# Kernel optimization log

Measured on AMD Instinct MI355X. Metric: run time of the kernel, lower is better.

Reference implementation:

```python
import jax, jax.numpy as jnp
import numpy as np

N_NODES = 100000
N_EDGES = 800000
N_GRAPHS = 64
D_IN = 128
D_H = 256
D_MID = 64
D_OUT = 3


def _sage_conv(x, src, dst, Wl, bl, Wr, n_nodes):
    # PyG SAGEConv (mean aggr): out = lin_l(mean_{j in N(i)} x_j) + lin_r(x_i)
    msg_sum = jax.ops.segment_sum(x[src], dst, num_segments=n_nodes)   # [N, d]
    deg = jax.ops.segment_sum(jnp.ones((src.shape[0],), x.dtype), dst,
                              num_segments=n_nodes)                     # [N]
    mean = msg_sum / jnp.maximum(deg, 1.0)[:, None]
    return mean @ Wl + bl + x @ Wr


def setup_inputs() -> dict:
    key = jax.random.key(0)
    ks = jax.random.split(key, 16)
    s = 0.05
    inp = {
        "x": jax.random.normal(ks[0], (N_NODES, D_IN), dtype=jnp.float32),
        "edge_index": jax.random.randint(ks[1], (2, N_EDGES), 0, N_NODES, dtype=jnp.int32),
        "batch": jnp.sort(jax.random.randint(ks[2], (N_NODES,), 0, N_GRAPHS, dtype=jnp.int32)),
        # conv1
        "W1l": jax.random.normal(ks[3], (D_IN, D_H), dtype=jnp.float32) * s,
        "b1l": jnp.zeros((D_H,), jnp.float32),
        "W1r": jax.random.normal(ks[4], (D_IN, D_H), dtype=jnp.float32) * s,
        # conv2
        "W2l": jax.random.normal(ks[5], (D_H, D_H), dtype=jnp.float32) * s,
        "b2l": jnp.zeros((D_H,), jnp.float32),
        "W2r": jax.random.normal(ks[6], (D_H, D_H), dtype=jnp.float32) * s,
        # conv3
        "W3l": jax.random.normal(ks[7], (D_H, D_H), dtype=jnp.float32) * s,
        "b3l": jnp.zeros((D_H,), jnp.float32),
        "W3r": jax.random.normal(ks[8], (D_H, D_H), dtype=jnp.float32) * s,
        # head
        "Wlin1": jax.random.normal(ks[9], (D_H, D_MID), dtype=jnp.float32) * s,
        "blin1": jnp.zeros((D_MID,), jnp.float32),
        "Wlin2": jax.random.normal(ks[10], (D_MID, D_OUT), dtype=jnp.float32) * s,
        "blin2": jnp.zeros((D_OUT,), jnp.float32),
    }
    return inp


def reference(x, edge_index, batch, W1l, b1l, W1r, W2l, b2l, W2r,
              W3l, b3l, W3r, Wlin1, blin1, Wlin2, blin2):
    src, dst = edge_index[0], edge_index[1]
    h = jnp.tanh(_sage_conv(x, src, dst, W1l, b1l, W1r, N_NODES))
    h = jnp.tanh(_sage_conv(h, src, dst, W2l, b2l, W2r, N_NODES))
    h = _sage_conv(h, src, dst, W3l, b3l, W3r, N_NODES)
    pooled = jax.ops.segment_max(h, batch, num_segments=N_GRAPHS)  # [G, 256]
    pooled = jnp.where(jnp.isneginf(pooled), 0.0, pooled)  # empty segments -> 0
    # dropout_rate = 0.0 -> identity
    h = jnp.tanh(pooled @ Wlin1 + blin1)
    return h @ Wlin2 + blin2
```

## Files before the change

### kernel.cpp

```cpp
#include <hip/hip_runtime.h>

#define N_NODES 100000
#define N_PAD   100224
#define N_EDGES 800000
#define N_GRAPHS 64
#define D_IN 128
#define D_H 256

typedef __attribute__((ext_vector_type(8))) short bf16x8;
typedef __attribute__((ext_vector_type(8))) unsigned short u16x8;
typedef __attribute__((ext_vector_type(4))) float f32x4;

__device__ inline float bf2f(unsigned short u) {
    union { unsigned u32; float f; } x;
    x.u32 = ((unsigned)u) << 16;
    return x.f;
}
__device__ inline unsigned short f2bf(float f) {
    unsigned u = __float_as_uint(f);
    if ((u & 0x7fffffffu) > 0x7f800000u) return (unsigned short)0x7fc0;
    unsigned r = ((u >> 16) & 1u) + 0x7fffu;
    return (unsigned short)((u + r) >> 16);
}

__device__ inline unsigned enc_f32(float f) {
    unsigned u = __float_as_uint(f);
    return (u & 0x80000000u) ? ~u : (u | 0x80000000u);
}
__device__ inline float dec_f32(unsigned u) {
    unsigned v = (u & 0x80000000u) ? (u & 0x7FFFFFFFu) : ~u;
    return __uint_as_float(v);
}
#define ENC_NEG_INF 0x007FFFFFu

#define GLOAD_LDS16(g, l)                                                     \
    __builtin_amdgcn_global_load_lds(                                         \
        (const __attribute__((address_space(1))) unsigned int*)(g),           \
        (__attribute__((address_space(3))) unsigned int*)(l), 16, 0, 0)

__global__ void k_init_counts(int* __restrict__ counts) {
    int i = blockIdx.x * blockDim.x + threadIdx.x;
    if (i < N_NODES) counts[i] = 0;
}

__global__ void k_count(const int* __restrict__ dst, int* __restrict__ counts) {
    int e = blockIdx.x * blockDim.x + threadIdx.x;
    if (e < N_EDGES) atomicAdd(&counts[dst[e]], 1);
}

__global__ void k_scan_block(const int* __restrict__ counts, int* __restrict__ excl,
                             int* __restrict__ bsums) {
    __shared__ int sh[1024];
    int tid = threadIdx.x;
    int i = blockIdx.x * 1024 + tid;
    int v = (i < N_NODES) ? counts[i] : 0;
    sh[tid] = v;
    __syncthreads();
    for (int off = 1; off < 1024; off <<= 1) {
        int t = (tid >= off) ? sh[tid - off] : 0;
        __syncthreads();
        sh[tid] += t;
        __syncthreads();
    }
    if (i < N_NODES) excl[i] = sh[tid] - v;
    if (tid == 1023) bsums[blockIdx.x] = sh[1023];
}

__global__ void k_scan_top(int* __restrict__ bsums, int nb) {
    __shared__ int sh[128];
    int tid = threadIdx.x;
    int v = (tid < nb) ? bsums[tid] : 0;
    sh[tid] = v;
    __syncthreads();
    for (int off = 1; off < 128; off <<= 1) {
        int t = (tid >= off) ? sh[tid - off] : 0;
        __syncthreads();
        sh[tid] += t;
        __syncthreads();
    }
    if (tid < nb) bsums[tid] = sh[tid] - v;
}

__global__ void k_scan_finish(const int* __restrict__ excl, const int* __restrict__ bsums,
                              const int* __restrict__ counts, int* __restrict__ indptr,
                              int* __restrict__ cursor, float* __restrict__ deg_inv) {
    int i = blockIdx.x * blockDim.x + threadIdx.x;
    if (i < N_NODES) {
        int p = excl[i] + bsums[i >> 10];
        indptr[i] = p;
        cursor[i] = p;
        deg_inv[i] = 1.0f / fmaxf((float)counts[i], 1.0f);
        if (i == 0) indptr[N_NODES] = N_EDGES;
    }
}

__global__ void k_fill(const int* __restrict__ src, const int* __restrict__ dst,
                       int* __restrict__ cursor, int* __restrict__ eidx) {
    int e = blockIdx.x * blockDim.x + threadIdx.x;
    if (e < N_EDGES) {
        int pos = atomicAdd(&cursor[dst[e]], 1);
        eidx[pos] = src[e];
    }
}

__global__ void k_x2bf(const float* __restrict__ x, unsigned short* __restrict__ hx) {
    const int total = N_NODES * D_IN / 4;
    for (int i = blockIdx.x * blockDim.x + threadIdx.x; i < total;
         i += gridDim.x * blockDim.x) {
        float4 v = reinterpret_cast<const float4*>(x)[i];
        ushort4 o;
        o.x = f2bf(v.x); o.y = f2bf(v.y); o.z = f2bf(v.z); o.w = f2bf(v.w);
        reinterpret_cast<ushort4*>(hx)[i] = o;
    }
}

template <int K>
__global__ void k_wt(const float* __restrict__ W, unsigned short* __restrict__ Wt) {
    int idx = blockIdx.x * blockDim.x + threadIdx.x;
    if (idx < K * 256) {
        int k = idx >> 8, n = idx & 255;
        Wt[n * K + k] = f2bf(W[idx]);
    }
}

template <bool IN_F32>
__global__ void k_agg(const void* __restrict__ hin, const int* __restrict__ indptr,
                      const int* __restrict__ eidx, const float* __restrict__ deg_inv,
                      unsigned short* __restrict__ mean) {
    constexpr int D = IN_F32 ? 128 : 256;
    constexpr int C = IN_F32 ? 4 : 8;
    int wid = (blockIdx.x * blockDim.x + threadIdx.x) >> 6;
    int lane = threadIdx.x & 63;
    int nw = (gridDim.x * blockDim.x) >> 6;
    int half = lane >> 5;
    int l = lane & 31;
    for (int node = wid; node < N_NODES; node += nw) {
        int beg = indptr[node], end = indptr[node + 1];
        float acc[C] = {};
        for (int e = beg + half; e < end; e += 2) {
            int s = eidx[e];
            if (IN_F32) {
                float4 v = reinterpret_cast<const float4*>((const float*)hin + (size_t)s * D)[l];
                acc[0] += v.x; acc[1] += v.y; acc[2] += v.z; acc[3] += v.w;
            } else {
                u16x8 v = reinterpret_cast<const u16x8*>((const unsigned short*)hin + (size_t)s * D)[l];
#pragma unroll
                for (int j = 0; j < 8; ++j) acc[j] += bf2f((unsigned short)v[j]);
            }
        }
#pragma unroll
        for (int i = 0; i < C; ++i) acc[i] += __shfl_xor(acc[i], 32);
        if (lane < 32) {
            float inv = deg_inv[node];
            unsigned short* orow = mean + (size_t)node * D;
            if (IN_F32) {
                ushort4 o;
                o.x = f2bf(acc[0] * inv); o.y = f2bf(acc[1] * inv);
                o.z = f2bf(acc[2] * inv); o.w = f2bf(acc[3] * inv);
                reinterpret_cast<ushort4*>(orow)[l] = o;
            } else {
                u16x8 o;
#pragma unroll
                for (int j = 0; j < 8; ++j) o[j] = f2bf(acc[j] * inv);
                reinterpret_cast<u16x8*>(orow)[l] = o;
            }
        }
    }
}

template <int K, bool TANH, bool POOL>
__global__ __launch_bounds__(512)
void k_xform(const unsigned short* __restrict__ A0, const unsigned short* __restrict__ A1,
             const unsigned short* __restrict__ Bt0, const unsigned short* __restrict__ Bt1,
             const float* __restrict__ bias,
             unsigned short* __restrict__ out,
             const int* __restrict__ batch, unsigned* __restrict__ pooled) {
    __shared__ unsigned short Al[128 * 32];
    __shared__ unsigned short Bl[256 * 32];

    const int tid = threadIdx.x;
    const int lane = tid & 63;
    const int wid = tid >> 6;
    const int wr = wid >> 2;
    const int wc = wid & 3;
    const int m0 = blockIdx.x * 128;

    f32x4 acc[4][4] = {};

    const int lrow = lane >> 2;
    const int lk8 = (lane & 3) * 8;

#pragma unroll
    for (int slab = 0; slab < 2; ++slab) {
        const unsigned short* As = slab ? A1 : A0;
        const unsigned short* Bs = slab ? Bt1 : Bt0;
        for (int k0 = 0; k0 < K; k0 += 32) {
            __syncthreads();
            GLOAD_LDS16(As + (size_t)(m0 + wid * 16 + lrow) * K + k0 + lk8, &Al[wid * 512]);
#pragma unroll
            for (int cc = 0; cc < 2; ++cc) {
                int c = wid * 2 + cc;
                GLOAD_LDS16(Bs + (size_t)(c * 16 + lrow) * K + k0 + lk8, &Bl[c * 512]);
            }
            asm volatile("s_waitcnt vmcnt(0)" ::: "memory");
            __syncthreads();

            bf16x8 af[4], bfr[4];
#pragma unroll
            for (int f = 0; f < 4; ++f) {
                af[f] = *reinterpret_cast<const bf16x8*>(
                    &Al[(wr * 64 + f * 16 + (lane & 15)) * 32 + (lane >> 4) * 8]);
                bfr[f] = *reinterpret_cast<const bf16x8*>(
                    &Bl[(wc * 64 + f * 16 + (lane & 15)) * 32 + (lane >> 4) * 8]);
            }
#pragma unroll
            for (int fi = 0; fi < 4; ++fi)
#pragma unroll
                for (int fj = 0; fj < 4; ++fj)
                    acc[fi][fj] = __builtin_amdgcn_mfma_f32_16x16x32_bf16(
                        af[fi], bfr[fj], acc[fi][fj], 0, 0, 0);
        }
    }

    const int rbase = m0 + wr * 64 + (lane >> 4) * 4;
    const int cbase = wc * 64 + (lane & 15);
    if (POOL) {
#pragma unroll
        for (int fj = 0; fj < 4; ++fj) {
            int col = cbase + fj * 16;
            float bcol = bias[col];
            int curg = -1;
            float curmax = 0.f;
#pragma unroll
            for (int fi = 0; fi < 4; ++fi) {
#pragma unroll
                for (int r = 0; r < 4; ++r) {
                    int row = rbase + fi * 16 + r;
                    if (row >= N_NODES) continue;
                    float v = acc[fi][fj][r] + bcol;
                    if (TANH) v = tanhf(v);
                    int g = batch[row];
                    if (g != curg) {
                        if (curg >= 0) atomicMax(&pooled[curg * 256 + col], enc_f32(curmax));
                        curg = g;
                        curmax = v;
                    } else {
                        curmax = fmaxf(curmax, v);
                    }
                }
            }
            if (curg >= 0) atomicMax(&pooled[curg * 256 + col], enc_f32(curmax));
        }
    } else {
#pragma unroll
        for (int fi = 0; fi < 4; ++fi) {
#pragma unroll
            for (int fj = 0; fj < 4; ++fj) {
                int col = cbase + fj * 16;
                float bcol = bias[col];
#pragma unroll
                for (int r = 0; r < 4; ++r) {
                    int row = rbase + fi * 16 + r;
                    if (row >= N_NODES) continue;
                    float v = acc[fi][fj][r] + bcol;
                    if (TANH) v = tanhf(v);
                    out[(size_t)row * 256 + col] = f2bf(v);
                }
            }
        }
    }
}

__global__ void k_pool_init(unsigned* __restrict__ pooled) {
    int i = blockIdx.x * blockDim.x + threadIdx.x;
    if (i < N_GRAPHS * 256) pooled[i] = ENC_NEG_INF;
}

__global__ void k_head(const unsigned* __restrict__ pooled,
                       const float* __restrict__ W1, const float* __restrict__ b1,
                       const float* __restrict__ W2, const float* __restrict__ b2,
                       float* __restrict__ out) {
    __shared__ float p[256];
    __shared__ float hm[64];
    int g = blockIdx.x;
    int t = threadIdx.x;
    for (int k = t; k < 256; k += 64) {
        unsigned u = pooled[g * 256 + k];
        p[k] = (u == ENC_NEG_INF) ? 0.0f : dec_f32(u);
    }
    __syncthreads();
    float a = b1[t];
    for (int k = 0; k < 256; ++k) a += p[k] * W1[k * 64 + t];
    hm[t] = tanhf(a);
    __syncthreads();
    if (t < 3) {
        float o = b2[t];
        for (int m = 0; m < 64; ++m) o += hm[m] * W2[m * 3 + t];
        out[g * 3 + t] = o;
    }
}

extern "C" void kernel_launch(void* const* d_in, const int* in_sizes, int n_in,
                              void* d_out, int out_size, void* d_ws, size_t ws_size,
                              hipStream_t stream) {
    const float* x     = (const float*)d_in[0];
    const int*   ei    = (const int*)d_in[1];
    const int*   src   = ei;
    const int*   dst   = ei + N_EDGES;
    const int*   batch = (const int*)d_in[2];
    const float* W1l = (const float*)d_in[3];
    const float* b1l = (const float*)d_in[4];
    const float* W1r = (const float*)d_in[5];
    const float* W2l = (const float*)d_in[6];
    const float* b2l = (const float*)d_in[7];
    const float* W2r = (const float*)d_in[8];
    const float* W3l = (const float*)d_in[9];
    const float* b3l = (const float*)d_in[10];
    const float* W3r = (const float*)d_in[11];
    const float* Wlin1 = (const float*)d_in[12];
    const float* blin1 = (const float*)d_in[13];
    const float* Wlin2 = (const float*)d_in[14];
    const float* blin2 = (const float*)d_in[15];
    float* out = (float*)d_out;

    char* base = (char*)d_ws;
    size_t off = 0;
    auto alloc = [&](size_t bytes) { char* p = base + off; off += (bytes + 255) & ~(size_t)255; return (void*)p; };
    int*   counts  = (int*)alloc(N_NODES * 4);
    int*   indptr  = (int*)alloc((N_NODES + 1) * 4);
    int*   cursor  = (int*)alloc(N_NODES * 4);
    int*   excl    = (int*)alloc(N_NODES * 4);
    int*   bsums   = (int*)alloc(128 * 4);
    float* deg_inv = (float*)alloc(N_NODES * 4);
    unsigned* pooled = (unsigned*)alloc(N_GRAPHS * 256 * 4);
    int*   eidx    = (int*)alloc(N_EDGES * 4);
    unsigned short* Wt1l = (unsigned short*)alloc(256 * 128 * 2);
    unsigned short* Wt1r = (unsigned short*)alloc(256 * 128 * 2);
    unsigned short* Wt2l = (unsigned short*)alloc(256 * 256 * 2);
    unsigned short* Wt2r = (unsigned short*)alloc(256 * 256 * 2);
    unsigned short* Wt3l = (unsigned short*)alloc(256 * 256 * 2);
    unsigned short* Wt3r = (unsigned short*)alloc(256 * 256 * 2);
    unsigned short* M   = (unsigned short*)alloc((size_t)N_PAD * 256 * 2);
    unsigned short* hA  = (unsigned short*)alloc((size_t)N_PAD * 256 * 2);
    unsigned short* hxB = (unsigned short*)alloc((size_t)N_PAD * 256 * 2);
    unsigned short* hx = hxB;
    unsigned short* hB = hxB;

    const int NB_SCAN = (N_NODES + 1023) / 1024;

    k_init_counts<<<(N_NODES + 255) / 256, 256, 0, stream>>>(counts);
    k_count<<<(N_EDGES + 255) / 256, 256, 0, stream>>>(dst, counts);
    k_scan_block<<<NB_SCAN, 1024, 0, stream>>>(counts, excl, bsums);
    k_scan_top<<<1, 128, 0, stream>>>(bsums, NB_SCAN);
    k_scan_finish<<<(N_NODES + 255) / 256, 256, 0, stream>>>(excl, bsums, counts, indptr, cursor, deg_inv);
    k_fill<<<(N_EDGES + 255) / 256, 256, 0, stream>>>(src, dst, cursor, eidx);

    k_x2bf<<<2048, 256, 0, stream>>>(x, hx);
    k_wt<128><<<(128 * 256 + 255) / 256, 256, 0, stream>>>(W1l, Wt1l);
    k_wt<128><<<(128 * 256 + 255) / 256, 256, 0, stream>>>(W1r, Wt1r);
    k_wt<256><<<(256 * 256 + 255) / 256, 256, 0, stream>>>(W2l, Wt2l);
    k_wt<256><<<(256 * 256 + 255) / 256, 256, 0, stream>>>(W2r, Wt2r);
    k_wt<256><<<(256 * 256 + 255) / 256, 256, 0, stream>>>(W3l, Wt3l);
    k_wt<256><<<(256 * 256 + 255) / 256, 256, 0, stream>>>(W3r, Wt3r);
    k_pool_init<<<(N_GRAPHS * 256 + 255) / 256, 256, 0, stream>>>(pooled);

    dim3 ggrid(782);

    k_agg<true><<<2048, 256, 0, stream>>>(x, indptr, eidx, deg_inv, M);
    k_xform<128, true, false><<<ggrid, 512, 0, stream>>>(M, hx, Wt1l, Wt1r, b1l, hA, nullptr, nullptr);

    k_agg<false><<<2048, 256, 0, stream>>>(hA, indptr, eidx, deg_inv, M);
    k_xform<256, true, false><<<ggrid, 512, 0, stream>>>(M, hA, Wt2l, Wt2r, b2l, hB, nullptr, nullptr);

    k_agg<false><<<2048, 256, 0, stream>>>(hB, indptr, eidx, deg_inv, M);
    k_xform<256, false, true><<<ggrid, 512, 0, stream>>>(M, hB, Wt3l, Wt3r, b3l, nullptr, batch, pooled);

    k_head<<<N_GRAPHS, 64, 0, stream>>>(pooled, Wlin1, blin1, Wlin2, blin2, out);
}
```

Before: 540.9 us.

## Double-buffer LDS tiles in transform GEMM to overlap global loads with MFMA

Result: slower. 612.3 us (+13.2%).

```diff
diff --git a/kernel.cpp b/kernel.cpp
--- a/kernel.cpp
+++ b/kernel.cpp
@@ -175,8 +175,8 @@
              const float* __restrict__ bias,
              unsigned short* __restrict__ out,
              const int* __restrict__ batch, unsigned* __restrict__ pooled) {
-    __shared__ unsigned short Al[128 * 32];
-    __shared__ unsigned short Bl[256 * 32];
+    __shared__ unsigned short Al[2][128 * 32];
+    __shared__ unsigned short Bl[2][256 * 32];
 
     const int tid = threadIdx.x;
     const int lane = tid & 63;
@@ -185,41 +185,57 @@
     const int wc = wid & 3;
     const int m0 = blockIdx.x * 128;
 
-    f32x4 acc[4][4] = {};
+    const int KS = K / 32;
+    const int NT = 2 * KS;
 
     const int lrow = lane >> 2;
     const int lk8 = (lane & 3) * 8;
 
-#pragma unroll
-    for (int slab = 0; slab < 2; ++slab) {
-        const unsigned short* As = slab ? A1 : A0;
-        const unsigned short* Bs = slab ? Bt1 : Bt0;
-        for (int k0 = 0; k0 < K; k0 += 32) {
-            __syncthreads();
-            GLOAD_LDS16(As + (size_t)(m0 + wid * 16 + lrow) * K + k0 + lk8, &Al[wid * 512]);
-#pragma unroll
-            for (int cc = 0; cc < 2; ++cc) {
-                int c = wid * 2 + cc;
-                GLOAD_LDS16(Bs + (size_t)(c * 16 + lrow) * K + k0 + lk8, &Bl[c * 512]);
-            }
+    f32x4 acc[4][4] = {};
+
+    auto stage = [&](int buf, int t) {
+        const unsigned short* As = (t < KS) ? A0 : A1;
+        const unsigned short* Bs = (t < KS) ? Bt0 : Bt1;
+        int k0 = (t < KS ? t : t - KS) * 32;
+        GLOAD_LDS16(As + (size_t)(m0 + wid * 16 + lrow) * K + k0 + lk8,
+                    &Al[buf][wid * 512]);
+#pragma unroll
+        for (int cc = 0; cc < 2; ++cc) {
+            int c = wid * 2 + cc;
+            GLOAD_LDS16(Bs + (size_t)(c * 16 + lrow) * K + k0 + lk8,
+                        &Bl[buf][c * 512]);
+        }
+    };
+
+    stage(0, 0);
+
+    for (int t = 0; t < NT; ++t) {
+        const int cur = t & 1;
+        if (t + 1 < NT) {
+            stage(cur ^ 1, t + 1);
+            asm volatile("s_waitcnt vmcnt(3)" ::: "memory");
+        } else {
             asm volatile("s_waitcnt vmcnt(0)" ::: "memory");
-            __syncthreads();
-
-            bf16x8 af[4], bfr[4];
-#pragma unroll
-            for (int f = 0; f < 4; ++f) {
-                af[f] = *reinterpret_cast<const bf16x8*>(
-                    &Al[(wr * 64 + f * 16 + (lane & 15)) * 32 + (lane >> 4) * 8]);
-                bfr[f] = *reinterpret_cast<const bf16x8*>(
-                    &Bl[(wc * 64 + f * 16 + (lane & 15)) * 32 + (lane >> 4) * 8]);
-            }
-#pragma unroll
-            for (int fi = 0; fi < 4; ++fi)
-#pragma unroll
-                for (int fj = 0; fj < 4; ++fj)
-                    acc[fi][fj] = __builtin_amdgcn_mfma_f32_16x16x32_bf16(
-                        af[fi], bfr[fj], acc[fi][fj], 0, 0, 0);
-        }
+        }
+        asm volatile("s_barrier" ::: "memory");
+
+        bf16x8 af[4], bfr[4];
+#pragma unroll
+        for (int f = 0; f < 4; ++f) {
+            af[f] = *reinterpret_cast<const bf16x8*>(
+                &Al[cur][(wr * 64 + f * 16 + (lane & 15)) * 32 + (lane >> 4) * 8]);
+            bfr[f] = *reinterpret_cast<const bf16x8*>(
+                &Bl[cur][(wc * 64 + f * 16 + (lane & 15)) * 32 + (lane >> 4) * 8]);
+        }
+        asm volatile("s_waitcnt lgkmcnt(0)" ::: "memory");
+        __builtin_amdgcn_sched_barrier(0);
+#pragma unroll
+        for (int fi = 0; fi < 4; ++fi)
+#pragma unroll
+            for (int fj = 0; fj < 4; ++fj)
+                acc[fi][fj] = __builtin_amdgcn_mfma_f32_16x16x32_bf16(
+                    af[fi], bfr[fj], acc[fi][fj], 0, 0, 0);
+        asm volatile("s_barrier" ::: "memory");
     }
 
     const int rbase = m0 + wr * 64 + (lane >> 4) * 4;
```
